# Kernel optimization log

Hardware: AMD Instinct MI355X
Metric: run time of the kernel (lower is better)

## Reference

```python
import jax, jax.numpy as jnp
import numpy as np

B, CIN, COUT, CLEV = 1, 128, 128, 64
H, W = 48, 160            # height//2**scale, width//2**scale (scale=2)
MIN_D, MAX_D = 0.1, 100.0


def conv3x3(x, w, b, mode):
    x = jnp.pad(x, ((0, 0), (0, 0), (1, 1), (1, 1)), mode=mode)
    y = jax.lax.conv_general_dilated(x, w, (1, 1), 'VALID',
                                     dimension_numbers=('NCHW', 'OIHW', 'NCHW'))
    return y + b[None, :, None, None]


def head(x, w1, b1, w2, b2):  # gaussian head: conv -> GELU -> conv, replicate pad
    return conv3x3(jax.nn.gelu(conv3x3(x, w1, b1, 'edge')), w2, b2, 'edge')


def convblock(x, w, b):  # ConvBlock: 3x3 conv (reflect pad) + ELU
    return jax.nn.elu(conv3x3(x, w, b, 'reflect'))


def to_pts(t):  # [B,C,H,W] -> [B,HW,C]
    return t.transpose(0, 2, 3, 1).reshape(t.shape[0], -1, t.shape[1])


def quat_to_rot(q):  # [N,4] (w,x,y,z) -> [N,3,3]
    w, x, y, z = q[:, 0], q[:, 1], q[:, 2], q[:, 3]
    return jnp.stack([1 - 2 * (y * y + z * z), 2 * (x * y - w * z), 2 * (x * z + w * y),
                      2 * (x * y + w * z), 1 - 2 * (x * x + z * z), 2 * (y * z - w * x),
                      2 * (x * z - w * y), 2 * (y * z + w * x), 1 - 2 * (x * x + y * y)],
                     axis=-1).reshape(-1, 3, 3)


def rasterize_one(pos, rot, scl, opa, feat, K):
    # depth-sort gaussians front-to-back
    order = jnp.argsort(pos[:, 2])
    pos, rot, scl, opa, feat = pos[order], rot[order], scl[order], opa[order], feat[order]
    x, y, z = pos[:, 0], pos[:, 1], pos[:, 2]
    fx, fy, cx, cy = K[0, 0], K[1, 1], K[0, 2], K[1, 2]
    u, v = fx * x / z + cx, fy * y / z + cy
    # 3D covariance Sigma = R S S^T R^T, projected with perspective Jacobian J
    M = quat_to_rot(rot) * scl[:, None, :]
    Sig = jnp.einsum('nij,nkj->nik', M, M)
    zer = jnp.zeros_like(z)
    J = jnp.stack([fx / z, zer, -fx * x / z ** 2,
                   zer, fy / z, -fy * y / z ** 2], axis=-1).reshape(-1, 2, 3)
    cov = jnp.einsum('nij,njk,nlk->nil', J, Sig, J)
    a = cov[:, 0, 0] + 0.3  # low-pass blur as in 3DGS
    bq = cov[:, 0, 1]
    c = cov[:, 1, 1] + 0.3
    det = a * c - bq * bq
    A, Bc, C = c / det, -bq / det, a / det  # conic (inverse 2D covariance)
    gy, gx = jnp.meshgrid(jnp.arange(H, dtype=pos.dtype),
                          jnp.arange(W, dtype=pos.dtype), indexing='ij')
    dx = gx.reshape(-1)[:, None] - u[None, :]  # [P,N]
    dy = gy.reshape(-1)[:, None] - v[None, :]
    power = -0.5 * (A[None] * dx * dx + C[None] * dy * dy) - Bc[None] * dx * dy
    alpha = jnp.where(power <= 0.,
                      jnp.clip(opa[None, :, 0] * jnp.exp(jnp.minimum(power, 0.)), 0., 0.99),
                      0.)
    l1m = jnp.log1p(-alpha)
    logT = jnp.cumsum(l1m, axis=1) - l1m  # exclusive transmittance along sorted axis
    wgt = alpha * jnp.exp(logT)           # [P,N]
    return (wgt @ feat).T.reshape(-1, H, W)  # [C,H,W]


def forward(init_feature, disp_init, inv_K, K,
            rot_w1, rot_b1, rot_w2, rot_b2,
            scl_w1, scl_b1, scl_w2, scl_b2,
            opa_w1, opa_b1, opa_w2, opa_b2,
            fl_w1, fl_b1, fl_w2, fl_b2, fr_w, fr_b):
    bs = init_feature.shape[0]
    # disp_to_depth
    scaled = 1. / MAX_D + (1. / MIN_D - 1. / MAX_D) * disp_init
    depth = jnp.clip(1. / scaled, MIN_D, MAX_D)
    # backproject depth to a point cloud
    gy, gx = jnp.meshgrid(jnp.arange(H, dtype=depth.dtype),
                          jnp.arange(W, dtype=depth.dtype), indexing='ij')
    pix = jnp.stack([gx.ravel(), gy.ravel(), jnp.ones(H * W, depth.dtype)], 0)  # [3,HW]
    cam = jnp.einsum('bij,jn->bin', inv_K[:, :3, :3], pix) * depth.reshape(bs, 1, -1)
    position = cam.transpose(0, 2, 1)  # [B,N,3]
    rot = head(init_feature, rot_w1, rot_b1, rot_w2, rot_b2)
    rot = rot / jnp.maximum(jnp.linalg.norm(rot, axis=1, keepdims=True), 1e-12)
    rotation = to_pts(rot)  # [B,N,4]
    scale = to_pts(jnp.abs(head(init_feature, scl_w1, scl_b1, scl_w2, scl_b2)))
    opacity = to_pts(jax.nn.sigmoid(head(init_feature, opa_w1, opa_b1, opa_w2, opa_b2)))
    gs_feat = to_pts(convblock(convblock(init_feature, fl_w1, fl_b1), fl_w2, fl_b2))
    lev = jax.vmap(rasterize_one)(position, rotation, scale, opacity, gs_feat, K)
    return convblock(lev, fr_w, fr_b)


def setup_inputs() -> dict:
    key = jax.random.key(0)
    ks = jax.random.split(key, 16)
    p = lambda i, shape: jax.random.normal(ks[i], shape, jnp.float32) * 0.05
    Kmat = np.array([[0.58 * W, 0, 0.5 * W, 0],
                     [0, 1.92 * H, 0.5 * H, 0],
                     [0, 0, 1, 0],
                     [0, 0, 0, 1]], dtype=np.float32)
    inv_K = np.linalg.inv(Kmat)
    return {
        'init_feature': jax.random.normal(ks[0], (B, CIN, H, W), jnp.float32),
        'disp_init': jax.random.uniform(ks[1], (B, 1, H, W), jnp.float32, 0.01, 0.99),
        'inv_K': jnp.tile(jnp.asarray(inv_K)[None], (B, 1, 1)),
        'K': jnp.tile(jnp.asarray(Kmat)[None], (B, 1, 1)),
        'rot_w1': p(2, (8, CIN, 3, 3)), 'rot_b1': jnp.zeros(8),
        'rot_w2': p(3, (4, 8, 3, 3)), 'rot_b2': jnp.zeros(4),
        'scl_w1': p(4, (6, CIN, 3, 3)), 'scl_b1': jnp.zeros(6),
        'scl_w2': p(5, (3, 6, 3, 3)), 'scl_b2': jnp.zeros(3),
        'opa_w1': p(6, (2, CIN, 3, 3)), 'opa_b1': jnp.zeros(2),
        'opa_w2': p(7, (1, 2, 3, 3)), 'opa_b2': jnp.zeros(1),
        'fl_w1': p(8, (CIN, CIN, 3, 3)), 'fl_b1': jnp.zeros(CIN),
        'fl_w2': p(9, (CLEV, CIN, 3, 3)), 'fl_b2': jnp.zeros(CLEV),
        'fr_w': p(10, (COUT, CLEV, 3, 3)), 'fr_b': jnp.zeros(COUT),
    }


def reference(init_feature, disp_init, inv_K, K, rot_w1, rot_b1, rot_w2, rot_b2,
              scl_w1, scl_b1, scl_w2, scl_b2, opa_w1, opa_b1, opa_w2, opa_b2,
              fl_w1, fl_b1, fl_w2, fl_b2, fr_w, fr_b):
    return forward(init_feature, disp_init, inv_K, K, rot_w1, rot_b1, rot_w2, rot_b2,
                   scl_w1, scl_b1, scl_w2, scl_b2, opa_w1, opa_b1, opa_w2, opa_b2,
                   fl_w1, fl_b1, fl_w2, fl_b2, fr_w, fr_b)
```

## Files before the change

kernel.cpp:

```cpp
#include <hip/hip_runtime.h>
#include <hip/hip_bf16.h>
#include <math.h>

#define Hh 48
#define Ww 160
#define NP 7680

using bf16 = __hip_bfloat16;
typedef __attribute__((ext_vector_type(8))) short v8s;
typedef __attribute__((ext_vector_type(4))) float v4f;

__device__ __forceinline__ float bfdec(unsigned short u) {
  return __uint_as_float(((unsigned)u) << 16);
}
__device__ __forceinline__ unsigned short bfenc(float x) {
  bf16 b = __float2bfloat16(x);
  return *(unsigned short*)&b;
}
__device__ __forceinline__ float ldany(const void* p, size_t i, int isbf) {
  return isbf ? bfdec(((const unsigned short*)p)[i]) : ((const float*)p)[i];
}

__device__ __forceinline__ int mapidx(int i, int n, int mode) {
  if (mode == 0) return i < 0 ? 0 : (i >= n ? n - 1 : i);
  return i < 0 ? -i : (i >= n ? 2 * n - 2 - i : i);
}

__device__ __forceinline__ float eluf(float v) { return v > 0.f ? v : expm1f(v); }
__device__ __forceinline__ float geluf(float v) {
  float c = v + 0.044715f * v * v * v;
  return 0.5f * v * (1.f + tanhf(0.7978845608028654f * c));
}

__global__ __launch_bounds__(256) void sniff_k(const unsigned short* __restrict__ w,
                                               int* __restrict__ flag) {
  __shared__ int cnt[256];
  int c = 0;
  for (int i = threadIdx.x; i < 2048; i += 256) {
    float a = fabsf(bfdec(w[i]));
    if (a > 1e-3f && a < 0.5f) c++;
  }
  cnt[threadIdx.x] = c;
  __syncthreads();
  for (int s = 128; s > 0; s >>= 1) {
    if (threadIdx.x < s) cnt[threadIdx.x] += cnt[threadIdx.x + s];
    __syncthreads();
  }
  if (threadIdx.x == 0) flag[0] = (cnt[0] > 1536) ? 1 : 0;
}

__global__ __launch_bounds__(256) void prep_all_k(const int* __restrict__ flag,
    const void* __restrict__ xsrc, unsigned short* __restrict__ xb,
    const void* disp, const void* invK, const void* K, const void* rw2,
    const void* rb2, const void* sw2, const void* sb2, const void* ow2, const void* ob2,
    const void* rb1, const void* sb1, const void* ob1, const void* fb1, const void* fb2,
    const void* frb, const void* rot_w1, const void* scl_w1, const void* opa_w1,
    const void* fl_w1, const void* fl_w2, const void* fr_w,
    float* __restrict__ dispf, float* __restrict__ smallf, float* __restrict__ biasf,
    unsigned short* __restrict__ a_h1, unsigned short* __restrict__ a_fl1,
    unsigned short* __restrict__ a_fl2, unsigned short* __restrict__ a_fr) {
  __shared__ float tile[32][33];
  const int f = *flag;
  if (blockIdx.x < 960) {
    const int bx = blockIdx.x;
    const int pb = (bx % 240) * 32, cb = (bx / 240) * 32;
#pragma unroll
    for (int pass = 0; pass < 4; pass++) {
      int ci = (threadIdx.x >> 5) + pass * 8, pl = threadIdx.x & 31;
      tile[ci][pl] = ldany(xsrc, (size_t)(cb + ci) * NP + pb + pl, f);
    }
    __syncthreads();
#pragma unroll
    for (int pass = 0; pass < 4; pass++) {
      int pl = (threadIdx.x >> 5) + pass * 8, ci = threadIdx.x & 31;
      xb[(size_t)(pb + pl) * 128 + cb + ci] = bfenc(tile[ci][pl]);
    }
    return;
  }
  int i = (blockIdx.x - 960) * 256 + threadIdx.x;
  if (i < 7680) { dispf[i] = ldany(disp, i, f); return; }
  i -= 7680;
  if (i < 508) {
    const void* src; int off;
    if (i < 16)       { src = invK; off = i; }
    else if (i < 32)  { src = K;    off = i - 16; }
    else if (i < 320) { src = rw2;  off = i - 32; }
    else if (i < 324) { src = rb2;  off = i - 320; }
    else if (i < 486) { src = sw2;  off = i - 324; }
    else if (i < 489) { src = sb2;  off = i - 486; }
    else if (i < 507) { src = ow2;  off = i - 489; }
    else              { src = ob2;  off = i - 507; }
    smallf[i] = ldany(src, off, f); return;
  }
  i -= 508;
  if (i < 336) {
    if (i < 8) biasf[i] = ldany(rb1, i, f);
    else if (i < 14) biasf[i] = ldany(sb1, i - 8, f);
    else if (i < 16) biasf[i] = ldany(ob1, i - 14, f);
    else if (i < 144) biasf[i] = ldany(fb1, i - 16, f);
    else if (i < 208) biasf[i] = ldany(fb2, i - 144, f);
    else biasf[i] = ldany(frb, i - 208, f);
    return;
  }
  i -= 336;
  if (i < 73728) {
    int co = i / 1152, rem = i - co * 1152;
    int t = rem >> 7, ci = rem & 127;
    float v = 0.f;
    if (co < 8) v = ldany(rot_w1, (size_t)co * 1152 + ci * 9 + t, f);
    else if (co < 14) v = ldany(scl_w1, (size_t)(co - 8) * 1152 + ci * 9 + t, f);
    else if (co < 16) v = ldany(opa_w1, (size_t)(co - 14) * 1152 + ci * 9 + t, f);
    a_h1[i] = bfenc(v); return;
  }
  i -= 73728;
  if (i < 147456) {
    int co = i / 1152, rem = i - co * 1152;
    int t = rem >> 7, ci = rem & 127;
    a_fl1[i] = bfenc(ldany(fl_w1, (size_t)co * 1152 + ci * 9 + t, f)); return;
  }
  i -= 147456;
  if (i < 73728) {
    int co = i / 1152, rem = i - co * 1152;
    int t = rem >> 7, ci = rem & 127;
    a_fl2[i] = bfenc(ldany(fl_w2, (size_t)co * 1152 + ci * 9 + t, f)); return;
  }
  i -= 73728;
  if (i < 73728) {
    int co = i / 576, rem = i - co * 576;
    int t = rem >> 6, ci = rem & 63;
    a_fr[i] = bfenc(ldany(fr_w, (size_t)co * 576 + ci * 9 + t, f));
    return;
  }
}

template<int OM, int PM, int ACT, bool GUARD, int KP, bool OPX>
__global__ __launch_bounds__(256) void gemm_conv4_k(const unsigned short* __restrict__ A,
    const unsigned short* __restrict__ X, const float* __restrict__ bias,
    void* __restrict__ out, const int* __restrict__ flag, int K, int glim) {
  __shared__ v8s As4[64][5];
  __shared__ v8s Bs4[64][5];
  __shared__ int off9s[64][9];
  const int tid = threadIdx.x;
  const int pxB = blockIdx.x * 64;
  const int coB = blockIdx.y * 64;
  if (tid < 64) {
    int p = pxB + tid;
    int h = p / Ww, w = p - h * Ww;
#pragma unroll
    for (int r = 0; r < 3; r++) {
      int hh = mapidx(h + r - 1, Hh, PM);
#pragma unroll
      for (int s = 0; s < 3; s++)
        off9s[tid][r * 3 + s] = hh * Ww + mapidx(w + s - 1, Ww, PM);
    }
  }
  const int lane = tid & 63, wv = tid >> 6;
  const int m16 = lane & 15, quad = lane >> 4;
  const int srow = tid >> 2, sg = tid & 3;
  v4f acc[4];
#pragma unroll
  for (int b = 0; b < 4; b++) acc[b] = (v4f){0.f, 0.f, 0.f, 0.f};
  __syncthreads();
  const int nIter = K >> 5;
  for (int it = 0; it < nIter; it++) {
    const int k0 = it << 5;
    {
      const unsigned short* ap = &A[(size_t)(coB + srow) * K + k0 + sg * 8];
      v8s av;
#pragma unroll
      for (int j = 0; j < 8; j++) av[j] = (short)ap[j];
      As4[srow][sg] = av;
    }
    {
      v8s bv;
      if (KP == 128) {
        int kk = k0 + sg * 8;
        int t = kk >> 7, c0 = kk & 127;
        const unsigned short* xp = &X[(size_t)off9s[srow][t] * 128 + c0];
#pragma unroll
        for (int j = 0; j < 8; j++) bv[j] = (short)xp[j];
      } else if (KP == 64) {
        int kk = k0 + sg * 8;
        int t = kk >> 6, c0 = kk & 63;
        const unsigned short* xp = &X[(size_t)off9s[srow][t] * 64 + c0];
#pragma unroll
        for (int j = 0; j < 8; j++) bv[j] = (short)xp[j];
      } else {
#pragma unroll
        for (int j = 0; j < 8; j++) {
          int k = k0 + sg * 8 + j;
          int ci = k / 9;
          int t = k - ci * 9;
          bv[j] = (short)X[(size_t)ci * NP + off9s[srow][t]];
        }
      }
      Bs4[srow][sg] = bv;
    }
    __syncthreads();
    v8s af = As4[wv * 16 + m16][quad];
    v8s bfr[4];
#pragma unroll
    for (int b = 0; b < 4; b++) bfr[b] = Bs4[b * 16 + m16][quad];
#pragma unroll
    for (int b = 0; b < 4; b++)
      acc[b] = __builtin_amdgcn_mfma_f32_16x16x32_bf16(af, bfr[b], acc[b], 0, 0, 0);
    __syncthreads();
  }
  const int obf = (OM == 2) ? *flag : (OM == 1);
#pragma unroll
  for (int b = 0; b < 4; b++) {
#pragma unroll
    for (int r = 0; r < 4; r++) {
      int co = coB + wv * 16 + quad * 4 + r;
      int px = pxB + b * 16 + m16;
      if (GUARD && co >= glim) continue;
      float bv = bias[GUARD ? (co & 15) : co];
      float v = acc[b][r] + bv;
      v = (ACT == 2) ? geluf(v) : eluf(v);
      size_t oi = OPX ? ((size_t)px * 128 + co) : ((size_t)co * NP + px);
      if (obf) ((unsigned short*)out)[oi] = bfenc(v);
      else ((float*)out)[oi] = v;
    }
  }
}

__global__ __launch_bounds__(256) void conv_fused1_k(
    const unsigned short* __restrict__ a_fl1, const unsigned short* __restrict__ a_h1,
    const unsigned short* __restrict__ X, const float* __restrict__ biasf,
    unsigned short* __restrict__ t1b, float* __restrict__ h1) {
  __shared__ v8s As4[64][5];
  __shared__ v8s Bs4[64][5];
  __shared__ int off9s[64][9];
  const int tid = threadIdx.x;
  const int zy = blockIdx.y;
  const bool ishead = (zy == 2);
  const int pm = ishead ? 0 : 1;
  const int pxB = blockIdx.x * 64;
  const int coB = ishead ? 0 : zy * 64;
  const unsigned short* A = ishead ? a_h1 : a_fl1;
  if (tid < 64) {
    int p = pxB + tid;
    int h = p / Ww, w = p - h * Ww;
#pragma unroll
    for (int r = 0; r < 3; r++) {
      int hh = mapidx(h + r - 1, Hh, pm);
#pragma unroll
      for (int s = 0; s < 3; s++)
        off9s[tid][r * 3 + s] = hh * Ww + mapidx(w + s - 1, Ww, pm);
    }
  }
  const int lane = tid & 63, wv = tid >> 6;
  const int m16 = lane & 15, quad = lane >> 4;
  const int srow = tid >> 2, sg = tid & 3;
  v4f acc[4];
#pragma unroll
  for (int b = 0; b < 4; b++) acc[b] = (v4f){0.f, 0.f, 0.f, 0.f};
  __syncthreads();
  for (int it = 0; it < 36; it++) {
    const int k0 = it << 5;
    {
      const unsigned short* ap = &A[(size_t)(coB + srow) * 1152 + k0 + sg * 8];
      v8s av;
#pragma unroll
      for (int j = 0; j < 8; j++) av[j] = (short)ap[j];
      As4[srow][sg] = av;
    }
    {
      int kk = k0 + sg * 8;
      int t = kk >> 7, c0 = kk & 127;
      const unsigned short* xp = &X[(size_t)off9s[srow][t] * 128 + c0];
      v8s bv;
#pragma unroll
      for (int j = 0; j < 8; j++) bv[j] = (short)xp[j];
      Bs4[srow][sg] = bv;
    }
    __syncthreads();
    v8s af = As4[wv * 16 + m16][quad];
    v8s bfr[4];
#pragma unroll
    for (int b = 0; b < 4; b++) bfr[b] = Bs4[b * 16 + m16][quad];
#pragma unroll
    for (int b = 0; b < 4; b++)
      acc[b] = __builtin_amdgcn_mfma_f32_16x16x32_bf16(af, bfr[b], acc[b], 0, 0, 0);
    __syncthreads();
  }
#pragma unroll
  for (int b = 0; b < 4; b++) {
#pragma unroll
    for (int r = 0; r < 4; r++) {
      int co = coB + wv * 16 + quad * 4 + r;
      int px = pxB + b * 16 + m16;
      if (ishead) {
        if (co < 16) h1[(size_t)co * NP + px] = geluf(acc[b][r] + biasf[co]);
      } else {
        t1b[(size_t)px * 128 + co] = bfenc(eluf(acc[b][r] + biasf[16 + co]));
      }
    }
  }
}

__global__ __launch_bounds__(64) void head2_prep_k(const float* __restrict__ h1,
    const float* __restrict__ smallf, const float* __restrict__ dispf,
    float* __restrict__ params, float* __restrict__ zbuf, int* __restrict__ rank) {
  const float* invK = smallf;
  const float* Km   = smallf + 16;
  const float* rw2  = smallf + 32;
  const float* rb2  = smallf + 320;
  const float* sw2  = smallf + 324;
  const float* sb2  = smallf + 486;
  const float* ow2  = smallf + 489;
  const float* ob2  = smallf + 507;
  int p = blockIdx.x * 64 + threadIdx.x;
  if (p >= NP) return;
  int hh = p / Ww, ww = p - hh * Ww;
  float racc[4], sacc[3], oacc;
#pragma unroll
  for (int i = 0; i < 4; i++) racc[i] = rb2[i];
#pragma unroll
  for (int i = 0; i < 3; i++) sacc[i] = sb2[i];
  oacc = ob2[0];
  for (int ci = 0; ci < 16; ci++) {
    float t9[9];
#pragma unroll
    for (int r = 0; r < 3; r++) {
      int rr = mapidx(hh + r - 1, Hh, 0);
#pragma unroll
      for (int s = 0; s < 3; s++) {
        int cc = mapidx(ww + s - 1, Ww, 0);
        t9[r * 3 + s] = h1[(size_t)ci * NP + rr * Ww + cc];
      }
    }
    if (ci < 8) {
      for (int co = 0; co < 4; co++)
#pragma unroll
        for (int k = 0; k < 9; k++)
          racc[co] = fmaf(t9[k], rw2[(co * 8 + ci) * 9 + k], racc[co]);
    } else if (ci < 14) {
      int c2 = ci - 8;
      for (int co = 0; co < 3; co++)
#pragma unroll
        for (int k = 0; k < 9; k++)
          sacc[co] = fmaf(t9[k], sw2[(co * 6 + c2) * 9 + k], sacc[co]);
    } else {
      int c2 = ci - 14;
#pragma unroll
      for (int k = 0; k < 9; k++)
        oacc = fmaf(t9[k], ow2[c2 * 9 + k], oacc);
    }
  }
  float nq = sqrtf(racc[0]*racc[0] + racc[1]*racc[1] + racc[2]*racc[2] + racc[3]*racc[3]);
  nq = fmaxf(nq, 1e-12f);
  float qw = racc[0] / nq, qx = racc[1] / nq, qy = racc[2] / nq, qz = racc[3] / nq;
  float s0 = fabsf(sacc[0]), s1 = fabsf(sacc[1]), s2 = fabsf(sacc[2]);
  float opa = 1.f / (1.f + __expf(-oacc));
  float d = dispf[p];
  float scaled = 0.01f + 9.99f * d;
  float depth = fminf(fmaxf(1.f / scaled, 0.1f), 100.f);
  float M00 = invK[0], M01 = invK[1], M02 = invK[2];
  float M10 = invK[4], M11 = invK[5], M12 = invK[6];
  float M20 = invK[8], M21 = invK[9], M22 = invK[10];
  float gxf = (float)ww, gyf = (float)hh;
  float X = (M00 * gxf + M01 * gyf + M02) * depth;
  float Y = (M10 * gxf + M11 * gyf + M12) * depth;
  float Z = (M20 * gxf + M21 * gyf + M22) * depth;
  float fxk = Km[0], fyk = Km[5];
  float cxk = Km[2], cyk = Km[6];
  float u = fxk * X / Z + cxk;
  float v = fyk * Y / Z + cyk;
  float R00 = 1.f - 2.f*(qy*qy + qz*qz), R01 = 2.f*(qx*qy - qw*qz), R02 = 2.f*(qx*qz + qw*qy);
  float R10 = 2.f*(qx*qy + qw*qz), R11 = 1.f - 2.f*(qx*qx + qz*qz), R12 = 2.f*(qy*qz - qw*qx);
  float R20 = 2.f*(qx*qz - qw*qy), R21 = 2.f*(qy*qz + qw*qx), R22 = 1.f - 2.f*(qx*qx + qy*qy);
  float M0a = R00*s0, M0b = R01*s1, M0c = R02*s2;
  float M1a = R10*s0, M1b = R11*s1, M1c = R12*s2;
  float M2a = R20*s0, M2b = R21*s1, M2c = R22*s2;
  float S00 = M0a*M0a + M0b*M0b + M0c*M0c;
  float S01 = M0a*M1a + M0b*M1b + M0c*M1c;
  float S02 = M0a*M2a + M0b*M2b + M0c*M2c;
  float S11 = M1a*M1a + M1b*M1b + M1c*M1c;
  float S12 = M1a*M2a + M1b*M2b + M1c*M2c;
  float S22 = M2a*M2a + M2b*M2b + M2c*M2c;
  float iz = 1.f / Z;
  float j00 = fxk * iz, j02 = -fxk * X * iz * iz;
  float j11 = fyk * iz, j12 = -fyk * Y * iz * iz;
  float c00 = j00*j00*S00 + 2.f*j00*j02*S02 + j02*j02*S22 + 0.3f;
  float c01 = j00*j11*S01 + j00*j12*S02 + j02*j11*S12 + j02*j12*S22;
  float c11 = j11*j11*S11 + 2.f*j11*j12*S12 + j12*j12*S22 + 0.3f;
  float det = c00 * c11 - c01 * c01;
  float idet = 1.f / det;
  float* pr = params + (size_t)p * 8;
  pr[0] = u; pr[1] = v; pr[2] = c11 * idet; pr[3] = -c01 * idet;
  pr[4] = c00 * idet; pr[5] = opa; pr[6] = Z; pr[7] = 0.f;
  zbuf[p] = Z;
  rank[p] = 0;
}

__global__ __launch_bounds__(256) void rank_count_k(const float* __restrict__ zbuf,
                                                    int* __restrict__ rank) {
  int i = blockIdx.x * 256 + threadIdx.x;
  int sid = blockIdx.y;
  float zi = zbuf[i];
  const float4* zv = (const float4*)(zbuf + sid * 960);
  int cnt = 0;
  for (int t = 0; t < 240; t++) {
    float4 z4 = zv[t];
    int jb = sid * 960 + t * 4;
    cnt += (z4.x < zi || (z4.x == zi && jb + 0 < i)) ? 1 : 0;
    cnt += (z4.y < zi || (z4.y == zi && jb + 1 < i)) ? 1 : 0;
    cnt += (z4.z < zi || (z4.z == zi && jb + 2 < i)) ? 1 : 0;
    cnt += (z4.w < zi || (z4.w == zi && jb + 3 < i)) ? 1 : 0;
  }
  atomicAdd(&rank[i], cnt);
}

__global__ __launch_bounds__(256) void scatter_k(const int* __restrict__ rank,
                                                 int* __restrict__ ord) {
  int i = blockIdx.x * 256 + threadIdx.x;
  ord[rank[i]] = i;
}

__global__ __launch_bounds__(64) void raster_seq_k(const int* __restrict__ ord,
    const float* __restrict__ params, const unsigned short* __restrict__ t2eb,
    unsigned short* __restrict__ levb) {
  __shared__ unsigned int Wl[64][17];
  __shared__ int ords[32];
  const int lane = threadIdx.x;
  const int m16 = lane & 15, quad = lane >> 4;
  const int pxB = blockIdx.x * 64;
  const int mypx = pxB + lane;
  const float px = (float)(mypx % Ww), py = (float)(mypx / Ww);
  float T = 1.f;
  v4f acc[4][4];
#pragma unroll
  for (int a = 0; a < 4; a++)
#pragma unroll
    for (int b = 0; b < 4; b++) acc[a][b] = (v4f){0.f, 0.f, 0.f, 0.f};
  for (int sub = 0; sub < NP / 32; sub++) {
    const int g0 = sub * 32;
    if (lane < 32) ords[lane] = ord[g0 + lane];
    __syncthreads();
    int myord[8];
#pragma unroll
    for (int j = 0; j < 8; j++) myord[j] = ords[quad * 8 + j];
    float al[32];
#pragma unroll
    for (int j = 0; j < 32; j++) {
      const float* pp = params + ((size_t)ords[j] << 3);
      float4 pa = *(const float4*)pp;
      float4 pb = *(const float4*)(pp + 4);
      float dx = px - pa.x, dy = py - pa.y;
      float power = -0.5f * (pa.z * dx * dx + pb.x * dy * dy) - pa.w * dx * dy;
      al[j] = fminf(pb.y * __expf(power), 0.99f);
    }
#pragma unroll
    for (int jj = 0; jj < 16; jj++) {
      float w0 = al[2 * jj] * T;     T *= 1.f - al[2 * jj];
      float w1 = al[2 * jj + 1] * T; T *= 1.f - al[2 * jj + 1];
      Wl[lane][jj] = (unsigned)bfenc(w0) | ((unsigned)bfenc(w1) << 16);
    }
    v8s af[4], bfr[4];
#pragma unroll
    for (int a = 0; a < 4; a++) {
      unsigned d0 = Wl[a * 16 + m16][quad * 4 + 0];
      unsigned d1 = Wl[a * 16 + m16][quad * 4 + 1];
      unsigned d2 = Wl[a * 16 + m16][quad * 4 + 2];
      unsigned d3 = Wl[a * 16 + m16][quad * 4 + 3];
      v8s t;
      t[0] = (short)(d0 & 0xffff); t[1] = (short)(d0 >> 16);
      t[2] = (short)(d1 & 0xffff); t[3] = (short)(d1 >> 16);
      t[4] = (short)(d2 & 0xffff); t[5] = (short)(d2 >> 16);
      t[6] = (short)(d3 & 0xffff); t[7] = (short)(d3 >> 16);
      af[a] = t;
    }
#pragma unroll
    for (int b = 0; b < 4; b++) {
      const unsigned short* fp = &t2eb[(size_t)(b * 16 + m16) * NP];
      v8s t;
#pragma unroll
      for (int j = 0; j < 8; j++) t[j] = (short)fp[myord[j]];
      bfr[b] = t;
    }
#pragma unroll
    for (int a = 0; a < 4; a++)
#pragma unroll
      for (int b = 0; b < 4; b++)
        acc[a][b] = __builtin_amdgcn_mfma_f32_16x16x32_bf16(af[a], bfr[b], acc[a][b], 0, 0, 0);
    if (__all(T < 1e-7f)) break;
    __syncthreads();
  }
#pragma unroll
  for (int a = 0; a < 4; a++) {
#pragma unroll
    for (int b = 0; b < 4; b++) {
#pragma unroll
      for (int r = 0; r < 4; r++) {
        levb[(size_t)(pxB + a * 16 + quad * 4 + r) * 64 + b * 16 + m16] =
            bfenc(acc[a][b][r]);
      }
    }
  }
}

extern "C" void kernel_launch(void* const* d_in, const int* in_sizes, int n_in,
                              void* d_out, int out_size, void* d_ws, size_t ws_size,
                              hipStream_t stream) {
  (void)in_sizes; (void)n_in; (void)out_size; (void)ws_size;
  const void* init_feature = d_in[0];
  const void* disp   = d_in[1];
  const void* invK   = d_in[2];
  const void* Km     = d_in[3];
  const void* rot_w1 = d_in[4];
  const void* rot_b1 = d_in[5];
  const void* rot_w2 = d_in[6];
  const void* rot_b2 = d_in[7];
  const void* scl_w1 = d_in[8];
  const void* scl_b1 = d_in[9];
  const void* scl_w2 = d_in[10];
  const void* scl_b2 = d_in[11];
  const void* opa_w1 = d_in[12];
  const void* opa_b1 = d_in[13];
  const void* opa_w2 = d_in[14];
  const void* opa_b2 = d_in[15];
  const void* fl_w1  = d_in[16];
  const void* fl_b1  = d_in[17];
  const void* fl_w2  = d_in[18];
  const void* fl_b2  = d_in[19];
  const void* fr_w   = d_in[20];
  const void* fr_b   = d_in[21];

  float* wsf = (float*)d_ws;
  int*   flag    = (int*)wsf;
  float* smallf  = wsf + 16;
  float* dispf   = wsf + 528;
  float* biasf   = wsf + 8208;
  unsigned short* a_h1  = (unsigned short*)(wsf + 8720);
  unsigned short* a_fl1 = (unsigned short*)(wsf + 45584);
  unsigned short* a_fl2 = (unsigned short*)(wsf + 119312);
  unsigned short* a_fr  = (unsigned short*)(wsf + 156176);
  unsigned short* xb    = (unsigned short*)(wsf + 193040);
  unsigned short* t1b   = (unsigned short*)(wsf + 684560);
  unsigned short* t2eb  = (unsigned short*)(wsf + 1176080);
  float* h1      = wsf + 1667600;
  float* params  = wsf + 1790480;
  unsigned short* levb = (unsigned short*)(wsf + 2896400);
  float* zbuf    = wsf + 3142160;
  int*   rank    = (int*)(wsf + 3149840);
  int*   ord     = (int*)(wsf + 3157520);

  sniff_k<<<1, 256, 0, stream>>>((const unsigned short*)fl_w1, flag);
  prep_all_k<<<2434, 256, 0, stream>>>(flag, init_feature, xb,
      disp, invK, Km, rot_w2, rot_b2, scl_w2, scl_b2, opa_w2, opa_b2,
      rot_b1, scl_b1, opa_b1, fl_b1, fl_b2, fr_b,
      rot_w1, scl_w1, opa_w1, fl_w1, fl_w2, fr_w,
      dispf, smallf, biasf, a_h1, a_fl1, a_fl2, a_fr);

  conv_fused1_k<<<dim3(120, 3), 256, 0, stream>>>(a_fl1, a_h1, xb, biasf, t1b, h1);
  gemm_conv4_k<1, 1, 1, false, 128, false><<<dim3(120, 1), 256, 0, stream>>>(
      a_fl2, t1b, biasf + 144, t2eb, flag, 1152, 64);
  head2_prep_k<<<120, 64, 0, stream>>>(h1, smallf, dispf, params, zbuf, rank);
  rank_count_k<<<dim3(30, 8), 256, 0, stream>>>(zbuf, rank);
  scatter_k<<<30, 256, 0, stream>>>(rank, ord);

  raster_seq_k<<<120, 64, 0, stream>>>(ord, params, t2eb, levb);
  gemm_conv4_k<2, 1, 1, false, 64, false><<<dim3(120, 2), 256, 0, stream>>>(
      a_fr, levb, biasf + 208, d_out, flag, 576, 128);
}
```

Baseline: 224.9 us.

## Fuse sniff into prep, merge fl2 GEMM with head2, collapse rank sort kernels

Removes the separate dtype-sniff kernel by having every prep block recompute the flag locally. A dedicated fl2 conv GEMM runs in the same launch as the head2 parameter preparation, split by block index. The three-kernel rank count, atomic add and scatter sort becomes one kernel that scans all depths per thread and writes the order directly. This cuts launch count and the atomic pass, at the cost of redundant sniff work in every prep block, a longer serial depth scan on only 30 blocks, and a hand-written GEMM that may be less tuned than the template it replaces.

```diff
diff --git a/kernel.cpp b/kernel.cpp
--- a/kernel.cpp
+++ b/kernel.cpp
@@ -32,9 +32,7 @@
   return 0.5f * v * (1.f + tanhf(0.7978845608028654f * c));
 }
 
-__global__ __launch_bounds__(256) void sniff_k(const unsigned short* __restrict__ w,
-                                               int* __restrict__ flag) {
-  __shared__ int cnt[256];
+__device__ __forceinline__ int sniff_local(const unsigned short* w, int* cnt) {
   int c = 0;
   for (int i = threadIdx.x; i < 2048; i += 256) {
     float a = fabsf(bfdec(w[i]));
@@ -46,10 +44,12 @@
     if (threadIdx.x < s) cnt[threadIdx.x] += cnt[threadIdx.x + s];
     __syncthreads();
   }
-  if (threadIdx.x == 0) flag[0] = (cnt[0] > 1536) ? 1 : 0;
-}
-
-__global__ __launch_bounds__(256) void prep_all_k(const int* __restrict__ flag,
+  int f = (cnt[0] > 1536) ? 1 : 0;
+  __syncthreads();
+  return f;
+}
+
+__global__ __launch_bounds__(256) void prep_all_k(int* __restrict__ flag,
     const void* __restrict__ xsrc, unsigned short* __restrict__ xb,
     const void* disp, const void* invK, const void* K, const void* rw2,
     const void* rb2, const void* sw2, const void* sb2, const void* ow2, const void* ob2,
@@ -60,7 +60,9 @@
     unsigned short* __restrict__ a_h1, unsigned short* __restrict__ a_fl1,
     unsigned short* __restrict__ a_fl2, unsigned short* __restrict__ a_fr) {
   __shared__ float tile[32][33];
-  const int f = *flag;
+  __shared__ int cnt[256];
+  const int f = sniff_local((const unsigned short*)fl_w1, cnt);
+  if (blockIdx.x == 0 && threadIdx.x == 0) flag[0] = f;
   if (blockIdx.x < 960) {
     const int bx = blockIdx.x;
     const int pb = (bx % 240) * 32, cb = (bx / 240) * 32;
@@ -299,9 +301,75 @@
   }
 }
 
-__global__ __launch_bounds__(64) void head2_prep_k(const float* __restrict__ h1,
-    const float* __restrict__ smallf, const float* __restrict__ dispf,
-    float* __restrict__ params, float* __restrict__ zbuf, int* __restrict__ rank) {
+__global__ __launch_bounds__(256) void fl2_head2_k(
+    const unsigned short* __restrict__ a_fl2, const unsigned short* __restrict__ t1b,
+    const float* __restrict__ biasf, unsigned short* __restrict__ t2eb,
+    const float* __restrict__ h1, const float* __restrict__ smallf,
+    const float* __restrict__ dispf, float* __restrict__ params,
+    float* __restrict__ zbuf) {
+  __shared__ v8s As4[64][5];
+  __shared__ v8s Bs4[64][5];
+  __shared__ int off9s[64][9];
+  const int tid = threadIdx.x;
+  if (blockIdx.x < 120) {
+    const int pxB = blockIdx.x * 64;
+    if (tid < 64) {
+      int p = pxB + tid;
+      int h = p / Ww, w = p - h * Ww;
+#pragma unroll
+      for (int r = 0; r < 3; r++) {
+        int hh = mapidx(h + r - 1, Hh, 1);
+#pragma unroll
+        for (int s = 0; s < 3; s++)
+          off9s[tid][r * 3 + s] = hh * Ww + mapidx(w + s - 1, Ww, 1);
+      }
+    }
+    const int lane = tid & 63, wv = tid >> 6;
+    const int m16 = lane & 15, quad = lane >> 4;
+    const int srow = tid >> 2, sg = tid & 3;
+    v4f acc[4];
+#pragma unroll
+    for (int b = 0; b < 4; b++) acc[b] = (v4f){0.f, 0.f, 0.f, 0.f};
+    __syncthreads();
+    for (int it = 0; it < 36; it++) {
+      const int k0 = it << 5;
+      {
+        const unsigned short* ap = &a_fl2[(size_t)srow * 1152 + k0 + sg * 8];
+        v8s av;
+#pragma unroll
+        for (int j = 0; j < 8; j++) av[j] = (short)ap[j];
+        As4[srow][sg] = av;
+      }
+      {
+        int kk = k0 + sg * 8;
+        int t = kk >> 7, c0 = kk & 127;
+        const unsigned short* xp = &t1b[(size_t)off9s[srow][t] * 128 + c0];
+        v8s bv;
+#pragma unroll
+        for (int j = 0; j < 8; j++) bv[j] = (short)xp[j];
+        Bs4[srow][sg] = bv;
+      }
+      __syncthreads();
+      v8s af = As4[wv * 16 + m16][quad];
+      v8s bfr[4];
+#pragma unroll
+      for (int b = 0; b < 4; b++) bfr[b] = Bs4[b * 16 + m16][quad];
+#pragma unroll
+      for (int b = 0; b < 4; b++)
+        acc[b] = __builtin_amdgcn_mfma_f32_16x16x32_bf16(af, bfr[b], acc[b], 0, 0, 0);
+      __syncthreads();
+    }
+#pragma unroll
+    for (int b = 0; b < 4; b++) {
+#pragma unroll
+      for (int r = 0; r < 4; r++) {
+        int co = wv * 16 + quad * 4 + r;
+        int px = pxB + b * 16 + m16;
+        t2eb[(size_t)co * NP + px] = bfenc(eluf(acc[b][r] + biasf[144 + co]));
+      }
+    }
+    return;
+  }
   const float* invK = smallf;
   const float* Km   = smallf + 16;
   const float* rw2  = smallf + 32;
@@ -310,7 +378,7 @@
   const float* sb2  = smallf + 486;
   const float* ow2  = smallf + 489;
   const float* ob2  = smallf + 507;
-  int p = blockIdx.x * 64 + threadIdx.x;
+  int p = (blockIdx.x - 120) * 256 + tid;
   if (p >= NP) return;
   int hh = p / Ww, ww = p - hh * Ww;
   float racc[4], sacc[3], oacc;
@@ -391,31 +459,23 @@
   pr[0] = u; pr[1] = v; pr[2] = c11 * idet; pr[3] = -c01 * idet;
   pr[4] = c00 * idet; pr[5] = opa; pr[6] = Z; pr[7] = 0.f;
   zbuf[p] = Z;
-  rank[p] = 0;
-}
-
-__global__ __launch_bounds__(256) void rank_count_k(const float* __restrict__ zbuf,
-                                                    int* __restrict__ rank) {
+}
+
+__global__ __launch_bounds__(256) void rank_sort_k(const float* __restrict__ zbuf,
+                                                   int* __restrict__ ord) {
   int i = blockIdx.x * 256 + threadIdx.x;
-  int sid = blockIdx.y;
   float zi = zbuf[i];
-  const float4* zv = (const float4*)(zbuf + sid * 960);
+  const float4* zv = (const float4*)zbuf;
   int cnt = 0;
-  for (int t = 0; t < 240; t++) {
+  for (int t = 0; t < NP / 4; t++) {
     float4 z4 = zv[t];
-    int jb = sid * 960 + t * 4;
+    int jb = t * 4;
     cnt += (z4.x < zi || (z4.x == zi && jb + 0 < i)) ? 1 : 0;
     cnt += (z4.y < zi || (z4.y == zi && jb + 1 < i)) ? 1 : 0;
     cnt += (z4.z < zi || (z4.z == zi && jb + 2 < i)) ? 1 : 0;
     cnt += (z4.w < zi || (z4.w == zi && jb + 3 < i)) ? 1 : 0;
   }
-  atomicAdd(&rank[i], cnt);
-}
-
-__global__ __launch_bounds__(256) void scatter_k(const int* __restrict__ rank,
-                                                 int* __restrict__ ord) {
-  int i = blockIdx.x * 256 + threadIdx.x;
-  ord[rank[i]] = i;
+  ord[cnt] = i;
 }
 
 __global__ __launch_bounds__(64) void raster_seq_k(const int* __restrict__ ord,
@@ -543,10 +603,8 @@
   float* params  = wsf + 1790480;
   unsigned short* levb = (unsigned short*)(wsf + 2896400);
   float* zbuf    = wsf + 3142160;
-  int*   rank    = (int*)(wsf + 3149840);
   int*   ord     = (int*)(wsf + 3157520);
 
-  sniff_k<<<1, 256, 0, stream>>>((const unsigned short*)fl_w1, flag);
   prep_all_k<<<2434, 256, 0, stream>>>(flag, init_feature, xb,
       disp, invK, Km, rot_w2, rot_b2, scl_w2, scl_b2, opa_w2, opa_b2,
       rot_b1, scl_b1, opa_b1, fl_b1, fl_b2, fr_b,
@@ -554,12 +612,9 @@
       dispf, smallf, biasf, a_h1, a_fl1, a_fl2, a_fr);
 
   conv_fused1_k<<<dim3(120, 3), 256, 0, stream>>>(a_fl1, a_h1, xb, biasf, t1b, h1);
-  gemm_conv4_k<1, 1, 1, false, 128, false><<<dim3(120, 1), 256, 0, stream>>>(
-      a_fl2, t1b, biasf + 144, t2eb, flag, 1152, 64);
-  head2_prep_k<<<120, 64, 0, stream>>>(h1, smallf, dispf, params, zbuf, rank);
-  rank_count_k<<<dim3(30, 8), 256, 0, stream>>>(zbuf, rank);
-  scatter_k<<<30, 256, 0, stream>>>(rank, ord);
-
+  fl2_head2_k<<<150, 256, 0, stream>>>(a_fl2, t1b, biasf, t2eb, h1, smallf,
+                                       dispf, params, zbuf);
+  rank_sort_k<<<30, 256, 0, stream>>>(zbuf, ord);
   raster_seq_k<<<120, 64, 0, stream>>>(ord, params, t2eb, levb);
   gemm_conv4_k<2, 1, 1, false, 64, false><<<dim3(120, 2), 256, 0, stream>>>(
       a_fr, levb, biasf + 208, d_out, flag, 576, 128);
```

New measurement: 464.4 us. 106% more time.
